# Optimization experiments

Hardware: AMD Instinct MI355X
Metric: run time of the kernel (lower is better)

Reference implementation:

```python
import jax, jax.numpy as jnp
import numpy as np

NUM_TREES = 256
DEPTH = 6
TREE_DIM = 2
INPUT_DIM = 256
BATCH = 2048


def sparsemax(x, axis=0):
    # Euclidean projection onto the simplex along `axis`.
    x = jnp.moveaxis(x, axis, -1)
    z = jnp.flip(jnp.sort(x, axis=-1), axis=-1)           # descending
    cz = jnp.cumsum(z, axis=-1)
    k = jnp.arange(1, x.shape[-1] + 1, dtype=x.dtype)
    support = (1.0 + k * z) > cz                          # boolean support set
    k_sel = jnp.sum(support, axis=-1, keepdims=True)      # |S(z)|
    tau = (jnp.take_along_axis(cz, k_sel - 1, axis=-1) - 1.0) / k_sel.astype(x.dtype)
    out = jnp.maximum(x - tau, 0.0)
    return jnp.moveaxis(out, -1, axis)


def sparsemoid(x):
    return jnp.clip(0.5 * x + 0.5, 0.0, 1.0)


def make_bin_codes(depth):
    idx = np.arange(2 ** depth)
    offs = 2 ** np.arange(depth)
    bc = ((idx[None, :] // offs[:, None]) % 2).astype(np.float32)  # [depth, 2^depth]
    return jnp.asarray(np.stack([bc, 1.0 - bc], axis=-1))          # [depth, 2^depth, 2]


def setup_inputs() -> dict:
    key = jax.random.key(0)
    ks = jax.random.split(key, 5)
    return {
        "inputs": jax.random.normal(ks[0], (BATCH, INPUT_DIM), dtype=jnp.float32),
        "feature_selection_logits": jax.random.normal(ks[1], (INPUT_DIM, NUM_TREES, DEPTH), dtype=jnp.float32),
        "feature_thresholds": jax.random.normal(ks[2], (NUM_TREES, DEPTH), dtype=jnp.float32) * 0.5,
        "log_temperatures": jax.random.normal(ks[3], (NUM_TREES, DEPTH), dtype=jnp.float32) * 0.1,
        "response": jax.random.normal(ks[4], (NUM_TREES, TREE_DIM, 2 ** DEPTH), dtype=jnp.float32),
    }


def reference(inputs, feature_selection_logits, feature_thresholds, log_temperatures, response):
    bin_codes_1hot = make_bin_codes(DEPTH)                                  # [d, 2^d, 2]
    selectors = sparsemax(feature_selection_logits, axis=0)                 # [i, n, d]
    feature_values = jnp.einsum('bi,ind->bnd', inputs, selectors)           # [b, n, d]
    tl = (feature_values - feature_thresholds) * jnp.exp(-log_temperatures) # [b, n, d]
    threshold_logits = jnp.stack([-tl, tl], axis=-1)                        # [b, n, d, 2]
    bins = sparsemoid(threshold_logits)                                     # [b, n, d, 2]
    bin_matches = jnp.einsum('bnds,dcs->bndc', bins, bin_codes_1hot)        # [b, n, d, 2^d]
    response_weights = jnp.prod(bin_matches, axis=-2)                       # [b, n, 2^d]
    out = jnp.einsum('bnc,ntc->bnt', response_weights, response)            # [b, n, tree_dim]
    return out.reshape(out.shape[0], -1)                                    # [b, n*tree_dim]
```

## Files before the change

### kernel.cpp

```cpp
#include <hip/hip_runtime.h>
#include <hip/hip_fp16.h>
#include <math.h>

#define NUM_TREES 256
#define DEPTH 6
#define TREE_DIM 2
#define INPUT_DIM 256
#define BATCH 2048
#define NLEAF 64
#define NCOLS (NUM_TREES * DEPTH)
#define KDIM INPUT_DIM

typedef _Float16 half8 __attribute__((ext_vector_type(8)));
typedef float floatx4 __attribute__((ext_vector_type(4)));

__global__ __launch_bounds__(256) void sparsemax_bisect(
    const float* __restrict__ fsl,
    const float* __restrict__ inputs,
    _Float16* __restrict__ selT,
    _Float16* __restrict__ inH)
{
    const int tid = threadIdx.x;
    {
        const int gid = blockIdx.x * 256 + tid;
        if (gid < (BATCH * INPUT_DIM) / 8) {
            const float4 v0 = ((const float4*)inputs)[gid * 2];
            const float4 v1 = ((const float4*)inputs)[gid * 2 + 1];
            half8 h;
            h[0] = (_Float16)v0.x; h[1] = (_Float16)v0.y;
            h[2] = (_Float16)v0.z; h[3] = (_Float16)v0.w;
            h[4] = (_Float16)v1.x; h[5] = (_Float16)v1.y;
            h[6] = (_Float16)v1.z; h[7] = (_Float16)v1.w;
            *(half8*)(inH + gid * 8) = h;
        }
    }

    const int lane = tid & 63;
    const int wave = tid >> 6;
    const int col  = blockIdx.x * 4 + wave;
    const int n = col / 6;
    const int d = col - n * 6;

    float x[4];
#pragma unroll
    for (int j = 0; j < 4; ++j)
        x[j] = fsl[(j * 64 + lane) * NCOLS + col];

    float mx = fmaxf(fmaxf(x[0], x[1]), fmaxf(x[2], x[3]));
#pragma unroll
    for (int off = 32; off > 0; off >>= 1)
        mx = fmaxf(mx, __shfl_xor(mx, off));

    float lo = mx - 1.0f, hi = mx;
    for (int it = 0; it < 16; ++it) {
        const float mid = 0.5f * (lo + hi);
        float s = fmaxf(x[0] - mid, 0.0f) + fmaxf(x[1] - mid, 0.0f)
                + fmaxf(x[2] - mid, 0.0f) + fmaxf(x[3] - mid, 0.0f);
#pragma unroll
        for (int off = 32; off > 0; off >>= 1)
            s += __shfl_xor(s, off);
        if (s > 1.0f) lo = mid; else hi = mid;
    }
    const float tau = 0.5f * (lo + hi);

    _Float16* dst = selT + (n * 8 + d) * KDIM;
#pragma unroll
    for (int j = 0; j < 4; ++j)
        dst[j * 64 + lane] = (_Float16)fmaxf(x[j] - tau, 0.0f);
}

#define BM 64
#define BN 64
#define BK 64
#define AP 72
#define BP 72
#define FVS 68

__global__ __launch_bounds__(256, 4) void odt_mfma_kernel(
    const _Float16* __restrict__ inH,
    const _Float16* __restrict__ selT,
    const float* __restrict__ thr,
    const float* __restrict__ logt,
    const float* __restrict__ resp,
    float* __restrict__ out)
{
    __shared__ union {
        struct {
            _Float16 A[BM][AP];
            _Float16 B[BN][BP];
        } s;
        float fv[BM][FVS];
    } u;
    __shared__ float respS[8 * TREE_DIM * NLEAF];

    const int tid = threadIdx.x;
    const int b0 = blockIdx.x * BM;
    const int treeBase = blockIdx.y * 8;
    const int colBase  = blockIdx.y * BN;

    ((float4*)respS)[tid] = ((const float4*)(resp + treeBase * TREE_DIM * NLEAF))[tid];

    const int lane = tid & 63;
    const int w    = tid >> 6;
    const int wm   = w >> 1, wn = w & 1;
    const int l16  = lane & 15, quad = lane >> 4;

    floatx4 acc[2][2];
#pragma unroll
    for (int mt = 0; mt < 2; ++mt)
#pragma unroll
        for (int nt = 0; nt < 2; ++nt)
            acc[mt][nt] = (floatx4){0.f, 0.f, 0.f, 0.f};

    const int srow = tid >> 2, sseg = tid & 3;

    for (int k0 = 0; k0 < KDIM; k0 += BK) {
        __syncthreads();
        {
            const _Float16* ag = inH + (b0 + srow) * KDIM + k0 + sseg * 16;
            const half8 a0 = *(const half8*)(ag);
            const half8 a1 = *(const half8*)(ag + 8);
            *(half8*)&u.s.A[srow][sseg * 16 + 0] = a0;
            *(half8*)&u.s.A[srow][sseg * 16 + 8] = a1;
            const _Float16* bg = selT + (colBase + srow) * KDIM + k0 + sseg * 16;
            const half8 bv0 = *(const half8*)(bg);
            const half8 bv1 = *(const half8*)(bg + 8);
            *(half8*)&u.s.B[srow][sseg * 16 + 0] = bv0;
            *(half8*)&u.s.B[srow][sseg * 16 + 8] = bv1;
        }
        __syncthreads();

#pragma unroll
        for (int h = 0; h < 2; ++h) {
            const half8 bf0 = *(const half8*)&u.s.B[wn * 32 + l16][quad * 8 + h * 32];
            const half8 bf1 = *(const half8*)&u.s.B[wn * 32 + 16 + l16][quad * 8 + h * 32];
            const half8 af0 = *(const half8*)&u.s.A[wm * 32 + l16][quad * 8 + h * 32];
            const half8 af1 = *(const half8*)&u.s.A[wm * 32 + 16 + l16][quad * 8 + h * 32];
            acc[0][0] = __builtin_amdgcn_mfma_f32_16x16x32_f16(af0, bf0, acc[0][0], 0, 0, 0);
            acc[0][1] = __builtin_amdgcn_mfma_f32_16x16x32_f16(af0, bf1, acc[0][1], 0, 0, 0);
            acc[1][0] = __builtin_amdgcn_mfma_f32_16x16x32_f16(af1, bf0, acc[1][0], 0, 0, 0);
            acc[1][1] = __builtin_amdgcn_mfma_f32_16x16x32_f16(af1, bf1, acc[1][1], 0, 0, 0);
        }
    }

    __syncthreads();

#pragma unroll
    for (int mt = 0; mt < 2; ++mt)
#pragma unroll
        for (int nt = 0; nt < 2; ++nt)
#pragma unroll
            for (int r = 0; r < 4; ++r)
                u.fv[wm * 32 + mt * 16 + quad * 4 + r][wn * 32 + nt * 16 + l16] = acc[mt][nt][r];
    __syncthreads();

#pragma unroll
    for (int p = 0; p < 2; ++p) {
        const int idx = tid + 256 * p;
        const int row = idx & 63;
        const int tl  = idx >> 6;
        const int n   = treeBase + tl;
        const float* f = &u.fv[row][tl * 8];

        float sd[DEPTH];
#pragma unroll
        for (int d = 0; d < DEPTH; ++d) {
            const float tlg = (f[d] - thr[n * DEPTH + d]) * __expf(-logt[n * DEPTH + d]);
            sd[d] = fminf(fmaxf(0.5f + 0.5f * tlg, 0.0f), 1.0f);
        }
        float wv[NLEAF / 2];
        wv[0] = 1.0f;
#pragma unroll
        for (int d = 0; d < 5; ++d) {
            const int sz = 1 << d;
#pragma unroll
            for (int c2 = 0; c2 < 16; ++c2) {
                if (c2 < sz) {
                    const float t = wv[c2];
                    wv[c2]      = t * sd[d];
                    wv[c2 + sz] = t * (1.0f - sd[d]);
                }
            }
        }
        const float* r0 = &respS[tl * TREE_DIM * NLEAF];
        float a0 = 0.f, b0s = 0.f, a1 = 0.f, b1s = 0.f;
#pragma unroll
        for (int c2 = 0; c2 < 32; ++c2) {
            a0  = fmaf(wv[c2], r0[c2], a0);
            b0s = fmaf(wv[c2], r0[c2 + 32], b0s);
            a1  = fmaf(wv[c2], r0[NLEAF + c2], a1);
            b1s = fmaf(wv[c2], r0[NLEAF + c2 + 32], b1s);
        }
        const float s5 = sd[5], s5b = 1.0f - sd[5];
        float2 o;
        o.x = s5 * a0 + s5b * b0s;
        o.y = s5 * a1 + s5b * b1s;
        *(float2*)(out + (b0 + row) * (NUM_TREES * TREE_DIM) + n * TREE_DIM) = o;
    }
}

extern "C" void kernel_launch(void* const* d_in, const int* in_sizes, int n_in,
                              void* d_out, int out_size, void* d_ws, size_t ws_size,
                              hipStream_t stream) {
    const float* inputs = (const float*)d_in[0];
    const float* fsl    = (const float*)d_in[1];
    const float* thr    = (const float*)d_in[2];
    const float* logt   = (const float*)d_in[3];
    const float* resp   = (const float*)d_in[4];
    float* out = (float*)d_out;
    _Float16* selT = (_Float16*)d_ws;
    _Float16* inH  = (_Float16*)((char*)d_ws + (1 << 20));

    hipLaunchKernelGGL(sparsemax_bisect, dim3(NCOLS / 4), dim3(256), 0, stream,
                       fsl, inputs, selT, inH);
    hipLaunchKernelGGL(odt_mfma_kernel, dim3(BATCH / BM, NUM_TREES / 8), dim3(256),
                       0, stream, inH, selT, thr, logt, resp, out);
}
```

Baseline: 90.38 us.

## Prefetch next K tile into registers, stage output via LDS, repad fv

The GEMM loop now loads the next K-slice of A and B into registers while the current tile is consumed, overlapping global latency with MFMA work. Output values are staged in a new shared buffer and written as float4 rows instead of scattered float2 stores, aiming for better coalescing. The fv padding changes from 68 to 67 to alter LDS bank mapping. The extra shared memory and prefetch registers may reduce occupancy.

```diff
diff --git a/kernel.cpp b/kernel.cpp
--- a/kernel.cpp
+++ b/kernel.cpp
@@ -74,7 +74,8 @@
 #define BK 64
 #define AP 72
 #define BP 72
-#define FVS 68
+#define FVS 67
+#define OSP 36
 
 __global__ __launch_bounds__(256, 4) void odt_mfma_kernel(
     const _Float16* __restrict__ inH,
@@ -92,6 +93,7 @@
         float fv[BM][FVS];
     } u;
     __shared__ float respS[8 * TREE_DIM * NLEAF];
+    __shared__ float outS[BM][OSP];
 
     const int tid = threadIdx.x;
     const int b0 = blockIdx.x * BM;
@@ -113,20 +115,26 @@
             acc[mt][nt] = (floatx4){0.f, 0.f, 0.f, 0.f};
 
     const int srow = tid >> 2, sseg = tid & 3;
-
+    const _Float16* aBase = inH  + (b0 + srow) * KDIM + sseg * 16;
+    const _Float16* bBase = selT + (colBase + srow) * KDIM + sseg * 16;
+
+    half8 pa0 = *(const half8*)(aBase);
+    half8 pa1 = *(const half8*)(aBase + 8);
+    half8 pb0 = *(const half8*)(bBase);
+    half8 pb1 = *(const half8*)(bBase + 8);
+
+#pragma unroll
     for (int k0 = 0; k0 < KDIM; k0 += BK) {
         __syncthreads();
-        {
-            const _Float16* ag = inH + (b0 + srow) * KDIM + k0 + sseg * 16;
-            const half8 a0 = *(const half8*)(ag);
-            const half8 a1 = *(const half8*)(ag + 8);
-            *(half8*)&u.s.A[srow][sseg * 16 + 0] = a0;
-            *(half8*)&u.s.A[srow][sseg * 16 + 8] = a1;
-            const _Float16* bg = selT + (colBase + srow) * KDIM + k0 + sseg * 16;
-            const half8 bv0 = *(const half8*)(bg);
-            const half8 bv1 = *(const half8*)(bg + 8);
-            *(half8*)&u.s.B[srow][sseg * 16 + 0] = bv0;
-            *(half8*)&u.s.B[srow][sseg * 16 + 8] = bv1;
+        *(half8*)&u.s.A[srow][sseg * 16 + 0] = pa0;
+        *(half8*)&u.s.A[srow][sseg * 16 + 8] = pa1;
+        *(half8*)&u.s.B[srow][sseg * 16 + 0] = pb0;
+        *(half8*)&u.s.B[srow][sseg * 16 + 8] = pb1;
+        if (k0 + BK < KDIM) {
+            pa0 = *(const half8*)(aBase + k0 + BK);
+            pa1 = *(const half8*)(aBase + k0 + BK + 8);
+            pb0 = *(const half8*)(bBase + k0 + BK);
+            pb1 = *(const half8*)(bBase + k0 + BK + 8);
         }
         __syncthreads();
 
@@ -183,19 +191,26 @@
             }
         }
         const float* r0 = &respS[tl * TREE_DIM * NLEAF];
-        float a0 = 0.f, b0s = 0.f, a1 = 0.f, b1s = 0.f;
+        float a0 = 0.f, c0 = 0.f, a1 = 0.f, c1 = 0.f;
 #pragma unroll
         for (int c2 = 0; c2 < 32; ++c2) {
-            a0  = fmaf(wv[c2], r0[c2], a0);
-            b0s = fmaf(wv[c2], r0[c2 + 32], b0s);
-            a1  = fmaf(wv[c2], r0[NLEAF + c2], a1);
-            b1s = fmaf(wv[c2], r0[NLEAF + c2 + 32], b1s);
+            a0 = fmaf(wv[c2], r0[c2], a0);
+            c0 = fmaf(wv[c2], r0[c2 + 32], c0);
+            a1 = fmaf(wv[c2], r0[NLEAF + c2], a1);
+            c1 = fmaf(wv[c2], r0[NLEAF + c2 + 32], c1);
         }
         const float s5 = sd[5], s5b = 1.0f - sd[5];
         float2 o;
-        o.x = s5 * a0 + s5b * b0s;
-        o.y = s5 * a1 + s5b * b1s;
-        *(float2*)(out + (b0 + row) * (NUM_TREES * TREE_DIM) + n * TREE_DIM) = o;
+        o.x = s5 * a0 + s5b * c0;
+        o.y = s5 * a1 + s5b * c1;
+        *(float2*)&outS[row][tl * 2] = o;
+    }
+    __syncthreads();
+
+    {
+        const int wrow = tid >> 2, wc = tid & 3;
+        const float4 v = *(const float4*)&outS[wrow][wc * 4];
+        *(float4*)(out + (b0 + wrow) * (NUM_TREES * TREE_DIM) + treeBase * 2 + wc * 4) = v;
     }
 }
 
```

Result: no change. 89.88 us (-0.6%).
